# Performance work log

Hardware: AMD Instinct MI355X
Metric: run time of the kernel (lower is better)

The kernel has to match this reference:

```python
import jax, jax.numpy as jnp
import numpy as np

B, T, D, H = 16, 1024, 512, 8
DH = D // H
NEG = jnp.float32(-2**32 + 1)


def setup_inputs() -> dict:
    key = jax.random.key(0)
    ks = jax.random.split(key, 9)
    s = 1.0 / np.sqrt(D)
    return {
        "queries": jax.random.normal(ks[0], (B, T, D), jnp.float32),
        "keys": jax.random.normal(ks[1], (B, T, D), jnp.float32),
        "value": jax.random.normal(ks[2], (B, T, D), jnp.float32),
        "Wq": jax.random.normal(ks[3], (D, D), jnp.float32) * s,
        "bq": jnp.zeros((D,), jnp.float32),
        "Wk": jax.random.normal(ks[4], (D, D), jnp.float32) * s,
        "bk": jnp.zeros((D,), jnp.float32),
        "Wv": jax.random.normal(ks[5], (D, D), jnp.float32) * s,
        "bv": jnp.zeros((D,), jnp.float32),
    }


def reference(queries, keys, value, Wq, bq, Wk, bk, Wv, bv):
    b, tq, d = queries.shape
    tk = keys.shape[1]
    # linear projections
    Q = queries @ Wq + bq   # [B,Tq,D]
    K = keys @ Wk + bk      # [B,Tk,D]
    V = value @ Wv + bv     # [B,Tk,D]
    # split heads: chunk along feature dim == reshape to [B,T,H,DH]
    Qh = Q.reshape(b, tq, H, DH)
    Kh = K.reshape(b, tk, H, DH)
    Vh = V.reshape(b, tk, H, DH)
    scores = jnp.einsum("bqhd,bkhd->bhqk", Qh, Kh) / jnp.sqrt(jnp.float32(DH))
    # key padding mask: rows of keys summing to 0 are padding
    key_mask = jnp.sign(jnp.abs(keys.sum(axis=-1)))      # [B,Tk]
    scores = jnp.where(key_mask[:, None, None, :] == 0, NEG, scores)
    # causal mask
    causal = jnp.tril(jnp.ones((tq, tk), jnp.float32))   # [Tq,Tk]
    scores = jnp.where(causal[None, None, :, :] == 0, NEG, scores)
    probs = jax.nn.softmax(scores, axis=-1)              # [B,H,Tq,Tk]
    # query padding mask (applied AFTER softmax, as in source)
    query_mask = jnp.sign(jnp.abs(queries.sum(axis=-1)))  # [B,Tq]
    probs = probs * query_mask[:, None, :, None]
    # dropout_rate=0.0 -> identity
    out = jnp.einsum("bhqk,bkhd->bqhd", probs, Vh).reshape(b, tq, d)
    return out + queries  # residual
```

## Files before the change

### kernel.cpp

```cpp
#include <hip/hip_runtime.h>
#include <hip/hip_bf16.h>

#define B_ 16
#define T_ 1024
#define D_ 512
#define H_ 8
#define M_ (B_ * T_)

typedef __attribute__((ext_vector_type(4))) float f32x4;
typedef __attribute__((ext_vector_type(8))) short bf16x8;
typedef __attribute__((ext_vector_type(4))) short bf16x4;

__device__ __forceinline__ void gld_lds16(const void* g, void* l) {
    __builtin_amdgcn_global_load_lds((const __attribute__((address_space(1))) void*)g,
                                     (__attribute__((address_space(3))) void*)l, 16, 0, 0);
}

__device__ __forceinline__ short f2bf(float f) {
    union { float f; unsigned u; } v; v.f = f;
    unsigned r = v.u + 0x7FFF + ((v.u >> 16) & 1);
    return (short)(r >> 16);
}

__global__ void prep_kernel(const float* __restrict__ q, const float* __restrict__ k,
                            const float* __restrict__ v,
                            const float* __restrict__ Wq, const float* __restrict__ Wk,
                            const float* __restrict__ Wv,
                            short* __restrict__ Xbf, short* __restrict__ WtAll,
                            float* __restrict__ qm, float* __restrict__ kb) {
    __shared__ float tile[64][65];
    const int t = threadIdx.x;
    const int mat = blockIdx.y;
    if (blockIdx.x < 64) {
        const float* W = (mat == 0) ? Wq : (mat == 1) ? Wk : Wv;
        short* Wt = WtAll + (size_t)mat * D_ * D_;
        const int kt = ((int)blockIdx.x >> 3) * 64;
        const int nt = ((int)blockIdx.x & 7) * 64;
#pragma unroll
        for (int i = 0; i < 4; ++i) {
            int idx = t + i * 256;
            int r = idx >> 4, c4 = idx & 15;
            float4 vv = *(const float4*)&W[(kt + r) * D_ + nt + c4 * 4];
            tile[r][c4 * 4 + 0] = vv.x; tile[r][c4 * 4 + 1] = vv.y;
            tile[r][c4 * 4 + 2] = vv.z; tile[r][c4 * 4 + 3] = vv.w;
        }
        __syncthreads();
#pragma unroll
        for (int i = 0; i < 2; ++i) {
            int idx = t + i * 256;
            int nr = idx >> 3, c8 = idx & 7;
            bf16x8 pk;
#pragma unroll
            for (int j = 0; j < 8; ++j) pk[j] = f2bf(tile[c8 * 8 + j][nr]);
            *(bf16x8*)&Wt[(nt + nr) * D_ + kt + c8 * 8] = pk;
        }
    } else {
        const int w = t >> 6, lane = t & 63;
        const int row = ((int)blockIdx.x - 64) * 4 + w;
        const float* X = (mat == 0) ? q : (mat == 1) ? k : v;
        short* O = Xbf + (size_t)mat * M_ * D_;
        const float4* p = (const float4*)&X[(size_t)row * D_];
        float4 v0 = p[lane], v1 = p[lane + 64];
        float s = v0.x + v0.y + v0.z + v0.w + v1.x + v1.y + v1.z + v1.w;
#pragma unroll
        for (int m = 1; m < 64; m <<= 1) s += __shfl_xor(s, m);
        bf16x4 p0, p1;
        p0[0] = f2bf(v0.x); p0[1] = f2bf(v0.y); p0[2] = f2bf(v0.z); p0[3] = f2bf(v0.w);
        p1[0] = f2bf(v1.x); p1[1] = f2bf(v1.y); p1[2] = f2bf(v1.z); p1[3] = f2bf(v1.w);
        *(bf16x4*)&O[(size_t)row * D_ + lane * 4] = p0;
        *(bf16x4*)&O[(size_t)row * D_ + 256 + lane * 4] = p1;
        if (lane == 0) {
            if (mat == 0) qm[row] = (s != 0.0f) ? 1.0f : 0.0f;
            else if (mat == 1) kb[row] = (s != 0.0f) ? 0.0f : -3e30f;
        }
    }
}

__global__ __launch_bounds__(256) void proj_gemm_bf(
    const short* __restrict__ Xbf, const short* __restrict__ WtAll,
    const float* __restrict__ bq, const float* __restrict__ bk, const float* __restrict__ bv,
    short* __restrict__ QKV, short* __restrict__ VtG) {
    __shared__ char As[16384];
    __shared__ char Bs[16384];
    const int t = threadIdx.x;
    const int u = blockIdx.x;
    const int wgid = (u & 7) * 192 + (u >> 3);
    const int mat = wgid >> 9;
    const int r = wgid & 511;
    const int m0 = (r >> 2) << 7, n0 = (r & 3) << 7;
    const short* X  = Xbf + (size_t)mat * M_ * D_;
    const short* Wt = WtAll + (size_t)mat * D_ * D_;
    const float* bias = (mat == 0) ? bq : (mat == 1) ? bk : bv;
    short* dst = QKV + (size_t)mat * M_ * D_;
    const int lane = t & 63, w = t >> 6;
    const int wr = w >> 1, wc = w & 1;
    const int cl = lane & 15, g = lane >> 4;

    const int r0 = t >> 3, c0 = ((t & 7) ^ (r0 & 7)) * 8;
    const short* sA = X  + (size_t)(m0 + r0) * D_ + c0;
    const short* sB = Wt + (size_t)(n0 + r0) * D_ + c0;

    f32x4 acc[4][4] = {};
#pragma unroll
    for (int i = 0; i < 4; ++i) {
        gld_lds16(sA + (size_t)(32 * i) * D_, As + t * 16 + i * 4096);
        gld_lds16(sB + (size_t)(32 * i) * D_, Bs + t * 16 + i * 4096);
    }
    for (int kt = 0; kt < D_; kt += 64) {
        __syncthreads();
#pragma unroll
        for (int ks = 0; ks < 2; ++ks) {
            bf16x8 a[4], b[4];
#pragma unroll
            for (int m = 0; m < 4; ++m)
                a[m] = *(const bf16x8*)(As + (wr * 64 + m * 16 + cl) * 128 + (((ks * 4 + g) ^ (cl & 7)) << 4));
#pragma unroll
            for (int n = 0; n < 4; ++n)
                b[n] = *(const bf16x8*)(Bs + (wc * 64 + n * 16 + cl) * 128 + (((ks * 4 + g) ^ (cl & 7)) << 4));
#pragma unroll
            for (int m = 0; m < 4; ++m)
#pragma unroll
                for (int n = 0; n < 4; ++n)
                    acc[m][n] = __builtin_amdgcn_mfma_f32_16x16x32_bf16(a[m], b[n], acc[m][n], 0, 0, 0);
        }
        __syncthreads();
        if (kt + 64 < D_) {
            const int k2 = kt + 64;
#pragma unroll
            for (int i = 0; i < 4; ++i) {
                gld_lds16(sA + (size_t)(32 * i) * D_ + k2, As + t * 16 + i * 4096);
                gld_lds16(sB + (size_t)(32 * i) * D_ + k2, Bs + t * 16 + i * 4096);
            }
        }
    }
    if (VtG != nullptr && mat == 2) {
        const int bb = m0 >> 10, tl0 = m0 & 1023;
#pragma unroll
        for (int n = 0; n < 4; ++n) {
            const int col = n0 + wc * 64 + n * 16 + cl;
            const int h = col >> 6, dh = col & 63;
            short* vrow = VtG + ((size_t)(bb * 8 + h) * 64 + dh) * T_;
            const float bv2 = bias[col];
#pragma unroll
            for (int m = 0; m < 4; ++m) {
                const int tl = tl0 + wr * 64 + m * 16 + g * 4;
                bf16x4 pk;
#pragma unroll
                for (int j = 0; j < 4; ++j) pk[j] = f2bf(acc[m][n][j] + bv2);
                *(bf16x4*)&vrow[tl] = pk;
            }
        }
    } else {
#pragma unroll
        for (int n = 0; n < 4; ++n) {
            int col = n0 + wc * 64 + n * 16 + cl;
            float bv2 = bias[col];
#pragma unroll
            for (int m = 0; m < 4; ++m) {
                int rowb = m0 + wr * 64 + m * 16 + g * 4;
#pragma unroll
                for (int j = 0; j < 4; ++j)
                    dst[(size_t)(rowb + j) * D_ + col] = f2bf(acc[m][n][j] + bv2);
            }
        }
    }
}

__global__ __launch_bounds__(256) void proj_gemm(
    const float* __restrict__ Xq, const float* __restrict__ Xk, const float* __restrict__ Xv,
    const short* __restrict__ WtAll,
    const float* __restrict__ bq, const float* __restrict__ bk, const float* __restrict__ bv,
    short* __restrict__ Qb, short* __restrict__ Kb, short* __restrict__ Vb) {
    __shared__ short As2[128][72];
    __shared__ short Bs2[128][72];
    const int t = threadIdx.x;
    const int mat = blockIdx.z;
    const float* X = (mat == 0) ? Xq : (mat == 1) ? Xk : Xv;
    const short* Wt = WtAll + (size_t)mat * D_ * D_;
    const float* bias = (mat == 0) ? bq : (mat == 1) ? bk : bv;
    short* dst = (mat == 0) ? Qb : (mat == 1) ? Kb : Vb;
    const int m0 = blockIdx.x * 128, n0 = blockIdx.y * 128;
    const int lane = t & 63, w = t >> 6;
    const int wr = w >> 1, wc = w & 1;
    const int cl = lane & 15, g = lane >> 4;
    f32x4 acc[4][4] = {};
    for (int kt = 0; kt < D_; kt += 64) {
#pragma unroll
        for (int i = 0; i < 8; ++i) {
            int idx = t + 256 * i;
            int r = idx >> 4, c4 = idx & 15;
            float4 v = *(const float4*)&X[(size_t)(m0 + r) * D_ + kt + c4 * 4];
            bf16x4 pk;
            pk[0] = f2bf(v.x); pk[1] = f2bf(v.y); pk[2] = f2bf(v.z); pk[3] = f2bf(v.w);
            *(bf16x4*)&As2[r][c4 * 4] = pk;
        }
#pragma unroll
        for (int i = 0; i < 4; ++i) {
            int idx = t + 256 * i;
            int r = idx >> 3, c8 = idx & 7;
            *(bf16x8*)&Bs2[r][c8 * 8] = *(const bf16x8*)&Wt[(size_t)(n0 + r) * D_ + kt + c8 * 8];
        }
        __syncthreads();
#pragma unroll
        for (int ks = 0; ks < 2; ++ks) {
            bf16x8 a[4], b[4];
#pragma unroll
            for (int m = 0; m < 4; ++m)
                a[m] = *(const bf16x8*)&As2[wr * 64 + m * 16 + cl][ks * 32 + g * 8];
#pragma unroll
            for (int n = 0; n < 4; ++n)
                b[n] = *(const bf16x8*)&Bs2[wc * 64 + n * 16 + cl][ks * 32 + g * 8];
#pragma unroll
            for (int m = 0; m < 4; ++m)
#pragma unroll
                for (int n = 0; n < 4; ++n)
                    acc[m][n] = __builtin_amdgcn_mfma_f32_16x16x32_bf16(a[m], b[n], acc[m][n], 0, 0, 0);
        }
        __syncthreads();
    }
#pragma unroll
    for (int n = 0; n < 4; ++n) {
        int col = n0 + wc * 64 + n * 16 + cl;
        float bv2 = bias[col];
#pragma unroll
        for (int m = 0; m < 4; ++m) {
            int rowb = m0 + wr * 64 + m * 16 + g * 4;
#pragma unroll
            for (int j = 0; j < 4; ++j)
                dst[(size_t)(rowb + j) * D_ + col] = f2bf(acc[m][n][j] + bv2);
        }
    }
}

__global__ void mask_kernel(const float* __restrict__ queries, const float* __restrict__ keys,
                            float* __restrict__ qm, float* __restrict__ kb) {
    const int w = threadIdx.x >> 6, lane = threadIdx.x & 63;
    const int row = blockIdx.x * 4 + w;
    const int which = blockIdx.y;
    const float* X = which ? keys : queries;
    const float4* p = (const float4*)&X[(size_t)row * D_];
    float s = 0.f;
#pragma unroll
    for (int i = 0; i < 2; ++i) {
        float4 v = p[lane + 64 * i];
        s += v.x + v.y + v.z + v.w;
    }
#pragma unroll
    for (int m = 1; m < 64; m <<= 1) s += __shfl_xor(s, m);
    if (lane == 0) {
        if (which) kb[row] = (s != 0.0f) ? 0.0f : -3e30f;
        else       qm[row] = (s != 0.0f) ? 1.0f : 0.0f;
    }
}

__global__ void vtrans_kernel(const short* __restrict__ Vb, short* __restrict__ VtG) {
    __shared__ short tile[64][72];
    const int t = threadIdx.x;
    const int kt = blockIdx.x & 15;
    const int h  = (blockIdx.x >> 4) & 7;
    const int b  = blockIdx.x >> 7;
#pragma unroll
    for (int i = 0; i < 2; ++i) {
        int idx = t + i * 256;
        int r = idx >> 3, c8 = idx & 7;
        *(bf16x8*)&tile[((r & 7) << 3) | (r >> 3)][c8 * 8] =
            *(const bf16x8*)&Vb[(size_t)(b * T_ + kt * 64 + r) * D_ + h * 64 + c8 * 8];
    }
    __syncthreads();
#pragma unroll
    for (int i = 0; i < 2; ++i) {
        int idx = t + i * 256;
        int d = idx >> 3, r8 = idx & 7;
        bf16x8 pk;
#pragma unroll
        for (int j = 0; j < 8; ++j) pk[j] = tile[(j << 3) | r8][d];
        *(bf16x8*)&VtG[(size_t)((b * 8 + h) * 64 + d) * T_ + kt * 64 + r8 * 8] = pk;
    }
}

__device__ __forceinline__ void qk_mfma(f32x4 (&s)[4], const char* Kl,
                                        const bf16x8 (&q)[2], int cl, int g) {
#pragma unroll
    for (int kc = 0; kc < 2; ++kc)
#pragma unroll
        for (int nc = 0; nc < 4; ++nc) {
            bf16x8 a = *(const bf16x8*)(Kl + (nc * 16 + cl) * 128 + (((kc * 4 + g) ^ (cl & 7)) << 4));
            s[nc] = __builtin_amdgcn_mfma_f32_16x16x32_bf16(a, q[kc], s[nc], 0, 0, 0);
        }
}

template <bool CAUSAL>
__device__ __forceinline__ void smax_pv(f32x4 (&s)[4], const f32x4 (&kb4)[4],
                                        f32x4 (&o)[4], float& m, float& l,
                                        int qmk, const char* Vl, int cl, int g) {
    const float csc = 0.125f * 1.44269504088896f;
    float pm = -3e30f;
#pragma unroll
    for (int nc = 0; nc < 4; ++nc)
#pragma unroll
        for (int j = 0; j < 4; ++j) {
            float v = fmaf(s[nc][j], csc, kb4[nc][j]);
            if (CAUSAL && (nc * 16 + g * 4 + j > qmk)) v = -3e30f;
            s[nc][j] = v;
            pm = fmaxf(pm, v);
        }
    pm = fmaxf(pm, __shfl_xor(pm, 16));
    pm = fmaxf(pm, __shfl_xor(pm, 32));
    if (__any(pm > m + 8.f)) {
        float mn = fmaxf(m, pm), cf;
        asm("v_exp_f32 %0, %1" : "=v"(cf) : "v"(m - mn));
        l *= cf;
        m = mn;
#pragma unroll
        for (int j = 0; j < 4; ++j) {
            float cfj = __shfl(cf, g * 4 + j);
#pragma unroll
            for (int dc = 0; dc < 4; ++dc) o[dc][j] *= cfj;
        }
    }
    float ps = 0.f;
#pragma unroll
    for (int nc = 0; nc < 4; ++nc)
#pragma unroll
        for (int j = 0; j < 4; ++j) {
            float p;
            asm("v_exp_f32 %0, %1" : "=v"(p) : "v"(s[nc][j] - m));
            s[nc][j] = p;
            ps += p;
        }
    l += ps;

    unsigned wp[4][2];
#pragma unroll
    for (int nc = 0; nc < 4; ++nc) {
        asm("v_cvt_pk_bf16_f32 %0, %1, %2" : "=v"(wp[nc][0]) : "v"(s[nc][0]), "v"(s[nc][1]));
        asm("v_cvt_pk_bf16_f32 %0, %1, %2" : "=v"(wp[nc][1]) : "v"(s[nc][2]), "v"(s[nc][3]));
    }
    const bool bp = (g & 1);
#pragma unroll
    for (int ks = 0; ks < 2; ++ks) {
        unsigned A0 = wp[2 * ks][0], A1 = wp[2 * ks][1];
        unsigned B0 = wp[2 * ks + 1][0], B1 = wp[2 * ks + 1][1];
        unsigned snd0 = bp ? A0 : B0, snd1 = bp ? A1 : B1;
        unsigned rcv0 = __shfl_xor(snd0, 16), rcv1 = __shfl_xor(snd1, 16);
        union { unsigned u[4]; bf16x8 v; } pa;
        pa.u[0] = bp ? rcv0 : A0;
        pa.u[1] = bp ? rcv1 : A1;
        pa.u[2] = bp ? B0 : rcv0;
        pa.u[3] = bp ? B1 : rcv1;
        const int vg = ks * 4 + (g & 1) * 2 + (g >> 1);
#pragma unroll
        for (int dc = 0; dc < 4; ++dc) {
            bf16x8 vv = *(const bf16x8*)(Vl + (dc * 16 + cl) * 128 + ((vg ^ (cl & 7)) << 4));
            o[dc] = __builtin_amdgcn_mfma_f32_16x16x32_bf16(pa.v, vv, o[dc], 0, 0, 0);
        }
    }
}

__global__ __launch_bounds__(256, 4) void attn_kernel(
    const short* __restrict__ Qb, const short* __restrict__ Kb,
    const short* __restrict__ VtG, const float* __restrict__ qmask,
    const float* __restrict__ kbias, const float* __restrict__ queries,
    float* __restrict__ out) {
    __shared__ char KV[2][2][8192];
    __shared__ float kbL[1024];
    const int t = threadIdx.x, lane = t & 63, w = t >> 6;
    const int cl = lane & 15, g = lane >> 4;
    const int u = blockIdx.x;
    const int wgid = (u & 7) * 128 + (u >> 3);
    const int pr = wgid & 7, h = (wgid >> 3) & 7, b = wgid >> 6;

    const int rS0 = t >> 3,  cS0 = ((t & 7) ^ (rS0 & 7)) * 8;
    const int t2 = t + 256;
    const int rS1 = t2 >> 3, cS1 = ((t2 & 7) ^ (rS1 & 7)) * 8;
    const short* kS0 = Kb  + ((size_t)(b * T_) + rS0) * D_ + h * 64 + cS0;
    const short* kS1 = Kb  + ((size_t)(b * T_) + rS1) * D_ + h * 64 + cS1;
    const short* vS0 = VtG + (size_t)((b * 8 + h) * 64 + rS0) * T_ + cS0;
    const short* vS1 = VtG + (size_t)((b * 8 + h) * 64 + rS1) * T_ + cS1;

    gld_lds16(kbias + b * T_ + t * 4, (char*)kbL + t * 16);

    int tb = 0;
#pragma unroll
    for (int pass = 0; pass < 2; ++pass) {
        const int qtile = pass ? pr : 15 - pr;
        const int nt = qtile + 1;
        const int qr = qtile * 64 + w * 16 + cl;

        bf16x8 qb[2];
#pragma unroll
        for (int kc = 0; kc < 2; ++kc)
            qb[kc] = *(const bf16x8*)&Qb[(size_t)(b * T_ + qr) * D_ + h * 64 + kc * 32 + g * 8];

        gld_lds16(kS0, &KV[tb][0][0]    + t * 16);
        gld_lds16(kS1, &KV[tb][0][4096] + t * 16);
        gld_lds16(vS0, &KV[tb][1][0]    + t * 16);
        gld_lds16(vS1, &KV[tb][1][4096] + t * 16);

        f32x4 o[4] = {};
        float m = -3e30f, l = 0.f;

        for (int it = 0; it < nt; ++it) {
            __syncthreads();

            f32x4 kb4[4];
#pragma unroll
            for (int nc = 0; nc < 4; ++nc)
                kb4[nc] = *(const f32x4*)((const char*)kbL + it * 256 + nc * 64 + g * 16);

            if (it + 1 < nt) {
                const int kt2 = (it + 1) * 64;
                char* db = &KV[tb ^ 1][0][0];
                gld_lds16(kS0 + (size_t)kt2 * D_, db + t * 16);
                gld_lds16(kS1 + (size_t)kt2 * D_, db + 4096 + t * 16);
                gld_lds16(vS0 + kt2, db + 8192 + t * 16);
                gld_lds16(vS1 + kt2, db + 8192 + 4096 + t * 16);
            }

            const char* Kl = &KV[tb][0][0];
            const char* Vl = &KV[tb][1][0];

            f32x4 s[4] = {};
            qk_mfma(s, Kl, qb, cl, g);
            if (it == nt - 1) smax_pv<true >(s, kb4, o, m, l, w * 16 + cl, Vl, cl, g);
            else              smax_pv<false>(s, kb4, o, m, l, 0,           Vl, cl, g);
            tb ^= 1;
        }

        float lt = l;
        lt += __shfl_xor(lt, 16);
        lt += __shfl_xor(lt, 32);
        float inv = 1.0f / lt;
#pragma unroll
        for (int j = 0; j < 4; ++j) {
            float linv = __shfl(inv, g * 4 + j);
            const int q = qtile * 64 + w * 16 + g * 4 + j;
            const float sc2 = linv * qmask[b * T_ + q];
            const size_t base = (size_t)(b * T_ + q) * D_ + h * 64;
#pragma unroll
            for (int dc = 0; dc < 4; ++dc) {
                const size_t idx = base + dc * 16 + cl;
                out[idx] = o[dc][j] * sc2 + queries[idx];
            }
        }
    }
}

extern "C" void kernel_launch(void* const* d_in, const int* in_sizes, int n_in,
                              void* d_out, int out_size, void* d_ws, size_t ws_size,
                              hipStream_t stream) {
    const float* queries = (const float*)d_in[0];
    const float* keys    = (const float*)d_in[1];
    const float* value   = (const float*)d_in[2];
    const float* Wq      = (const float*)d_in[3];
    const float* bq      = (const float*)d_in[4];
    const float* Wk      = (const float*)d_in[5];
    const float* bk      = (const float*)d_in[6];
    const float* Wv      = (const float*)d_in[7];
    const float* bv      = (const float*)d_in[8];
    float* out = (float*)d_out;

    char* ws = (char*)d_ws;
    const size_t WT_SZ  = (size_t)D_ * D_ * 2;
    const size_t XB_SZ  = (size_t)M_ * D_ * 2;
    const size_t MASKS  = 2 * (size_t)M_ * 4;

    const size_t NEED_FULL = 3 * WT_SZ + 7 * XB_SZ + MASKS;
    const size_t NEED_MID  = 3 * WT_SZ + 6 * XB_SZ + MASKS;

    if (ws_size >= NEED_FULL) {
        short* WtAll = (short*)(ws);
        short* Xbf   = (short*)(ws + 3 * WT_SZ);
        short* QKV   = (short*)(ws + 3 * WT_SZ + 3 * XB_SZ);
        short* Qb = QKV, *Kb = QKV + M_ * D_;
        short* VtG   = (short*)(ws + 3 * WT_SZ + 6 * XB_SZ);
        float* qm    = (float*)(ws + 3 * WT_SZ + 7 * XB_SZ);
        float* kb    = qm + M_;

        prep_kernel<<<dim3(64 + M_ / 4, 3), 256, 0, stream>>>(
            queries, keys, value, Wq, Wk, Wv, Xbf, WtAll, qm, kb);
        proj_gemm_bf<<<1536, 256, 0, stream>>>(Xbf, WtAll, bq, bk, bv, QKV, VtG);
        attn_kernel<<<1024, 256, 0, stream>>>(Qb, Kb, VtG, qm, kb, queries, out);
    } else if (ws_size >= NEED_MID) {
        short* WtAll = (short*)(ws);
        short* Xbf   = (short*)(ws + 3 * WT_SZ);
        short* QKV   = (short*)(ws + 3 * WT_SZ + 3 * XB_SZ);
        short* Qb = QKV, *Kb = QKV + M_ * D_, *Vb = QKV + 2 * (size_t)M_ * D_;
        short* VtG   = Xbf;
        float* qm    = (float*)(ws + 3 * WT_SZ + 6 * XB_SZ);
        float* kb    = qm + M_;

        prep_kernel<<<dim3(64 + M_ / 4, 3), 256, 0, stream>>>(
            queries, keys, value, Wq, Wk, Wv, Xbf, WtAll, qm, kb);
        proj_gemm_bf<<<1536, 256, 0, stream>>>(Xbf, WtAll, bq, bk, bv, QKV, nullptr);
        vtrans_kernel<<<B_ * H_ * (T_ / 64), 256, 0, stream>>>(Vb, VtG);
        attn_kernel<<<1024, 256, 0, stream>>>(Qb, Kb, VtG, qm, kb, queries, out);
    } else {
        short* WtAll = (short*)(ws);
        short* Qb  = (short*)(ws + 3 * WT_SZ);
        short* Kb  = (short*)(ws + 3 * WT_SZ + XB_SZ);
        short* Vb  = (short*)(ws + 3 * WT_SZ + 2 * XB_SZ);
        short* VtG = (short*)(ws + 3 * WT_SZ + 3 * XB_SZ);
        float* qm  = (float*)(ws + 3 * WT_SZ + 4 * XB_SZ);
        float* kb  = qm + M_;

        prep_kernel<<<dim3(64, 3), 256, 0, stream>>>(
            queries, keys, value, Wq, Wk, Wv, nullptr, WtAll, qm, kb);
        mask_kernel<<<dim3(M_ / 4, 2), 256, 0, stream>>>(queries, keys, qm, kb);
        proj_gemm<<<dim3(M_ / 128, D_ / 128, 3), 256, 0, stream>>>(
            queries, keys, value, WtAll, bq, bk, bv, Qb, Kb, Vb);
        vtrans_kernel<<<B_ * H_ * (T_ / 64), 256, 0, stream>>>(Vb, VtG);
        attn_kernel<<<1024, 256, 0, stream>>>(Qb, Kb, VtG, qm, kb, queries, out);
    }
}
```

Before: 102.2 us.

## Split attention into one q-tile per block, single-buffer K/V, raise occupancy

The attention kernel previously processed two paired causal q-tiles per block (15-pr and pr) for load balance, with double-buffered K/V prefetch in LDS and a kbias copy staged into LDS. Now each block handles one q-tile, the grid doubles to 2048, LDS drops to a single 16KB K/V buffer, and launch bounds ask for 8 blocks per SM. The key bias is read straight from global. This trades the copy/compute overlap of double buffering (an extra barrier now waits on each load) and the balanced pairing for more resident waves hiding latency. Blocks are also unequal in work.

```diff
diff --git a/kernel.cpp b/kernel.cpp
--- a/kernel.cpp
+++ b/kernel.cpp
@@ -357,18 +357,20 @@
     }
 }
 
-__global__ __launch_bounds__(256, 4) void attn_kernel(
+__global__ __launch_bounds__(256, 8) void attn_kernel(
     const short* __restrict__ Qb, const short* __restrict__ Kb,
     const short* __restrict__ VtG, const float* __restrict__ qmask,
     const float* __restrict__ kbias, const float* __restrict__ queries,
     float* __restrict__ out) {
-    __shared__ char KV[2][2][8192];
-    __shared__ float kbL[1024];
+    __shared__ char KV[2][8192];
     const int t = threadIdx.x, lane = t & 63, w = t >> 6;
     const int cl = lane & 15, g = lane >> 4;
     const int u = blockIdx.x;
-    const int wgid = (u & 7) * 128 + (u >> 3);
-    const int pr = wgid & 7, h = (wgid >> 3) & 7, b = wgid >> 6;
+    const int wgid = (u & 7) * 256 + (u >> 3);
+    const int qtile = 15 - (wgid & 15);
+    const int h = (wgid >> 4) & 7, b = wgid >> 7;
+    const int nt = qtile + 1;
+    const int qr = qtile * 64 + w * 16 + cl;
 
     const int rS0 = t >> 3,  cS0 = ((t & 7) ^ (rS0 & 7)) * 8;
     const int t2 = t + 256;
@@ -377,71 +379,50 @@
     const short* kS1 = Kb  + ((size_t)(b * T_) + rS1) * D_ + h * 64 + cS1;
     const short* vS0 = VtG + (size_t)((b * 8 + h) * 64 + rS0) * T_ + cS0;
     const short* vS1 = VtG + (size_t)((b * 8 + h) * 64 + rS1) * T_ + cS1;
-
-    gld_lds16(kbias + b * T_ + t * 4, (char*)kbL + t * 16);
-
-    int tb = 0;
-#pragma unroll
-    for (int pass = 0; pass < 2; ++pass) {
-        const int qtile = pass ? pr : 15 - pr;
-        const int nt = qtile + 1;
-        const int qr = qtile * 64 + w * 16 + cl;
-
-        bf16x8 qb[2];
-#pragma unroll
-        for (int kc = 0; kc < 2; ++kc)
-            qb[kc] = *(const bf16x8*)&Qb[(size_t)(b * T_ + qr) * D_ + h * 64 + kc * 32 + g * 8];
-
-        gld_lds16(kS0, &KV[tb][0][0]    + t * 16);
-        gld_lds16(kS1, &KV[tb][0][4096] + t * 16);
-        gld_lds16(vS0, &KV[tb][1][0]    + t * 16);
-        gld_lds16(vS1, &KV[tb][1][4096] + t * 16);
-
-        f32x4 o[4] = {};
-        float m = -3e30f, l = 0.f;
-
-        for (int it = 0; it < nt; ++it) {
-            __syncthreads();
-
-            f32x4 kb4[4];
-#pragma unroll
-            for (int nc = 0; nc < 4; ++nc)
-                kb4[nc] = *(const f32x4*)((const char*)kbL + it * 256 + nc * 64 + g * 16);
-
-            if (it + 1 < nt) {
-                const int kt2 = (it + 1) * 64;
-                char* db = &KV[tb ^ 1][0][0];
-                gld_lds16(kS0 + (size_t)kt2 * D_, db + t * 16);
-                gld_lds16(kS1 + (size_t)kt2 * D_, db + 4096 + t * 16);
-                gld_lds16(vS0 + kt2, db + 8192 + t * 16);
-                gld_lds16(vS1 + kt2, db + 8192 + 4096 + t * 16);
-            }
-
-            const char* Kl = &KV[tb][0][0];
-            const char* Vl = &KV[tb][1][0];
-
-            f32x4 s[4] = {};
-            qk_mfma(s, Kl, qb, cl, g);
-            if (it == nt - 1) smax_pv<true >(s, kb4, o, m, l, w * 16 + cl, Vl, cl, g);
-            else              smax_pv<false>(s, kb4, o, m, l, 0,           Vl, cl, g);
-            tb ^= 1;
-        }
-
-        float lt = l;
-        lt += __shfl_xor(lt, 16);
-        lt += __shfl_xor(lt, 32);
-        float inv = 1.0f / lt;
-#pragma unroll
-        for (int j = 0; j < 4; ++j) {
-            float linv = __shfl(inv, g * 4 + j);
-            const int q = qtile * 64 + w * 16 + g * 4 + j;
-            const float sc2 = linv * qmask[b * T_ + q];
-            const size_t base = (size_t)(b * T_ + q) * D_ + h * 64;
-#pragma unroll
-            for (int dc = 0; dc < 4; ++dc) {
-                const size_t idx = base + dc * 16 + cl;
-                out[idx] = o[dc][j] * sc2 + queries[idx];
-            }
+    const float* kbp = kbias + b * T_;
+
+    bf16x8 qb[2];
+#pragma unroll
+    for (int kc = 0; kc < 2; ++kc)
+        qb[kc] = *(const bf16x8*)&Qb[(size_t)(b * T_ + qr) * D_ + h * 64 + kc * 32 + g * 8];
+
+    f32x4 o[4] = {};
+    float m = -3e30f, l = 0.f;
+
+    for (int it = 0; it < nt; ++it) {
+        __syncthreads();
+        const int kt2 = it * 64;
+        gld_lds16(kS0 + (size_t)kt2 * D_, &KV[0][0] + t * 16);
+        gld_lds16(kS1 + (size_t)kt2 * D_, &KV[0][4096] + t * 16);
+        gld_lds16(vS0 + kt2, &KV[1][0] + t * 16);
+        gld_lds16(vS1 + kt2, &KV[1][4096] + t * 16);
+        __syncthreads();
+
+        f32x4 kb4[4];
+#pragma unroll
+        for (int nc = 0; nc < 4; ++nc)
+            kb4[nc] = *(const f32x4*)&kbp[it * 64 + nc * 16 + g * 4];
+
+        f32x4 s[4] = {};
+        qk_mfma(s, &KV[0][0], qb, cl, g);
+        if (it == nt - 1) smax_pv<true >(s, kb4, o, m, l, w * 16 + cl, &KV[1][0], cl, g);
+        else              smax_pv<false>(s, kb4, o, m, l, 0,           &KV[1][0], cl, g);
+    }
+
+    float lt = l;
+    lt += __shfl_xor(lt, 16);
+    lt += __shfl_xor(lt, 32);
+    float inv = 1.0f / lt;
+#pragma unroll
+    for (int j = 0; j < 4; ++j) {
+        float linv = __shfl(inv, g * 4 + j);
+        const int q = qtile * 64 + w * 16 + g * 4 + j;
+        const float sc2 = linv * qmask[b * T_ + q];
+        const size_t base = (size_t)(b * T_ + q) * D_ + h * 64;
+#pragma unroll
+        for (int dc = 0; dc < 4; ++dc) {
+            const size_t idx = base + dc * 16 + cl;
+            out[idx] = o[dc][j] * sc2 + queries[idx];
         }
     }
 }
@@ -480,7 +461,7 @@
         prep_kernel<<<dim3(64 + M_ / 4, 3), 256, 0, stream>>>(
             queries, keys, value, Wq, Wk, Wv, Xbf, WtAll, qm, kb);
         proj_gemm_bf<<<1536, 256, 0, stream>>>(Xbf, WtAll, bq, bk, bv, QKV, VtG);
-        attn_kernel<<<1024, 256, 0, stream>>>(Qb, Kb, VtG, qm, kb, queries, out);
+        attn_kernel<<<2048, 256, 0, stream>>>(Qb, Kb, VtG, qm, kb, queries, out);
     } else if (ws_size >= NEED_MID) {
         short* WtAll = (short*)(ws);
         short* Xbf   = (short*)(ws + 3 * WT_SZ);
@@ -494,7 +475,7 @@
             queries, keys, value, Wq, Wk, Wv, Xbf, WtAll, qm, kb);
         proj_gemm_bf<<<1536, 256, 0, stream>>>(Xbf, WtAll, bq, bk, bv, QKV, nullptr);
         vtrans_kernel<<<B_ * H_ * (T_ / 64), 256, 0, stream>>>(Vb, VtG);
-        attn_kernel<<<1024, 256, 0, stream>>>(Qb, Kb, VtG, qm, kb, queries, out);
+        attn_kernel<<<2048, 256, 0, stream>>>(Qb, Kb, VtG, qm, kb, queries, out);
     } else {
         short* WtAll = (short*)(ws);
         short* Qb  = (short*)(ws + 3 * WT_SZ);
@@ -510,6 +491,6 @@
         proj_gemm<<<dim3(M_ / 128, D_ / 128, 3), 256, 0, stream>>>(
             queries, keys, value, WtAll, bq, bk, bv, Qb, Kb, Vb);
         vtrans_kernel<<<B_ * H_ * (T_ / 64), 256, 0, stream>>>(Vb, VtG);
-        attn_kernel<<<1024, 256, 0, stream>>>(Qb, Kb, VtG, qm, kb, queries, out);
-    }
-}
+        attn_kernel<<<2048, 256, 0, stream>>>(Qb, Kb, VtG, qm, kb, queries, out);
+    }
+}
```

Result: slower. 336.3 us (+228.9%).
